# Performance work log

Hardware: AMD Instinct MI355X
Metric: run time of the kernel (lower is better)

## Reference

```python
import jax, jax.numpy as jnp
import numpy as np

B = 2
DIMS = ((41, 800, 800), (21, 400, 400), (11, 200, 200), (6, 100, 100))  # (D,H,W)=(z,y,x) per level
VS = ((0.1, 0.1, 0.2), (0.2, 0.2, 0.4), (0.4, 0.4, 0.8), (0.8, 0.8, 1.6))  # (vx,vy,vz)
OFFSET = (0.0, -40.0, -3.0)  # world offset (x,y,z)
BN_EPS = 1e-3

OFFS27 = jnp.array([[z, y, x] for z in (-1, 0, 1) for y in (-1, 0, 1) for x in (-1, 0, 1)], jnp.int32)

# ---------------- numpy-side input construction ----------------

def _np_downsample(coords, out_dims):
    # active output sites of SparseConv3d(k=3, s=2, p=1): in = 2*o - 1 + kd, kd in 0..2
    outs = []
    for kz in range(3):
        for ky in range(3):
            for kx in range(3):
                o = coords[:, 1:] + 1 - np.array([kz, ky, kx])
                ok = (o % 2 == 0).all(1)
                oc = o // 2
                ok &= (oc >= 0).all(1)
                ok &= (oc[:, 0] < out_dims[0]) & (oc[:, 1] < out_dims[1]) & (oc[:, 2] < out_dims[2])
                outs.append(np.concatenate([coords[ok, :1], oc[ok]], 1))
    return np.unique(np.concatenate(outs, 0), axis=0).astype(np.int32)


def _make_coords(rng):
    per_batch = []
    D0, H0, W0 = DIMS[0]
    for b in range(B):
        nc = 120
        centers = np.stack([rng.integers(3, D0 - 4, nc), rng.integers(5, H0 - 6, nc), rng.integers(5, W0 - 6, nc)], 1)
        offs = rng.integers(-3, 4, (nc, 40, 3))
        p = np.clip((centers[:, None, :] + offs).reshape(-1, 3), 0, np.array(DIMS[0]) - 1)
        p = np.unique(p, axis=0)  # sorted lexicographically == sorted by linear key
        per_batch.append(np.concatenate([np.full((len(p), 1), b), p], 1))
    return np.concatenate(per_batch, 0).astype(np.int32)


def setup_inputs():
    rng = np.random.default_rng(0)
    coords0 = _make_coords(rng)
    coords1 = _np_downsample(coords0, DIMS[1])
    coords2 = _np_downsample(coords1, DIMS[2])
    coords3 = _np_downsample(coords2, DIMS[3])
    n = coords0.shape[0]
    c = coords0.astype(np.float64)
    x = OFFSET[0] + (c[:, 3] + 0.5) * VS[0][0] + rng.uniform(-0.04, 0.04, n)
    y = OFFSET[1] + (c[:, 2] + 0.5) * VS[0][1] + rng.uniform(-0.04, 0.04, n)
    z = OFFSET[2] + (c[:, 1] + 0.5) * VS[0][2] + rng.uniform(-0.08, 0.08, n)
    vf = np.stack([x, y, z, rng.uniform(0.0, 1.0, n)], 1).astype(np.float32)

    def conv_w(k, cin, cout):
        return (rng.standard_normal((k, cin, cout)) / np.sqrt(k * cin)).astype(np.float32)

    def bn_p(ch):
        return np.stack([1.0 + 0.05 * rng.standard_normal(ch), 0.05 * rng.standard_normal(ch)], 0).astype(np.float32)

    inp = dict(voxel_features=vf, coords0=coords0, coords1=coords1, coords2=coords2, coords3=coords3,
               w00=conv_w(27, 4, 16), b00=bn_p(16), w01=conv_w(27, 16, 16), b01=bn_p(16),
               wd0=conv_w(27, 16, 32), bd0=bn_p(32),
               w10=conv_w(27, 32, 32), b10=bn_p(32), w11=conv_w(27, 32, 32), b11=bn_p(32),
               wd1=conv_w(27, 32, 64), bd1=bn_p(64),
               w20=conv_w(27, 64, 64), b20=bn_p(64), w21=conv_w(27, 64, 64), b21=bn_p(64), w22=conv_w(27, 64, 64), b22=bn_p(64),
               wd2=conv_w(27, 64, 64), bd2=bn_p(64),
               w30=conv_w(27, 64, 64), b30=bn_p(64), w31=conv_w(27, 64, 64), b31=bn_p(64), w32=conv_w(27, 64, 64), b32=bn_p(64),
               we=(rng.standard_normal((64, 64)) / 8.0).astype(np.float32), be=bn_p(64),
               fc_w=(rng.standard_normal((64, 160)) / np.sqrt(160.0)).astype(np.float32),
               cls_w=(rng.standard_normal((1, 64)) / 8.0).astype(np.float32),
               reg_w=(rng.standard_normal((3, 64)) / 8.0).astype(np.float32))
    return {k: jnp.asarray(v) for k, v in inp.items()}

# ---------------- jax sparse-conv primitives ----------------

def _key(c, dims):
    D, H, W = dims
    return ((c[:, 0] * D + c[:, 1]) * H + c[:, 2]) * W + c[:, 3]


def _gather(nb_b, nb, feats, keys_sorted, dims):
    # nb: (N,27,3) candidate (z,y,x); gather rows of feats via sorted-key lookup, zeros if absent
    D, H, W = dims
    inb = (nb[..., 0] >= 0) & (nb[..., 0] < D) & (nb[..., 1] >= 0) & (nb[..., 1] < H) & (nb[..., 2] >= 0) & (nb[..., 2] < W)
    nbc = jnp.clip(nb, 0, jnp.array(dims, jnp.int32) - 1)
    qk = ((nb_b * D + nbc[..., 0]) * H + nbc[..., 1]) * W + nbc[..., 2]
    pos = jnp.clip(jnp.searchsorted(keys_sorted, qk), 0, keys_sorted.shape[0] - 1)
    found = inb & (keys_sorted[pos] == qk)
    return jnp.where(found[..., None], feats[pos], 0.0)


def _subm(feats, coords, keys, dims, w):
    nb = coords[:, None, 1:] + OFFS27[None]
    g = _gather(coords[:, None, 0], nb, feats, keys, dims)  # (N,27,Cin)
    return jnp.einsum('nkc,kco->no', g, w)


def _stride(feats, in_keys, in_dims, coords_out, w):
    nb = coords_out[:, None, 1:] * 2 + OFFS27[None]  # in = 2*o - 1 + kd
    g = _gather(coords_out[:, None, 0], nb, feats, in_keys, in_dims)
    return jnp.einsum('nkc,kco->no', g, w)


def _bn_relu(x, p):
    # train-mode BatchNorm1d over active voxels (biased var), eps=1e-3
    m = x.mean(0)
    v = jnp.mean((x - m) ** 2, 0)
    return jax.nn.relu((x - m) * jax.lax.rsqrt(v + BN_EPS) * p[0] + p[1])


def _t2p(coords, vs):
    c = coords.astype(jnp.float32)
    x = OFFSET[0] + (c[:, 3] + 0.5) * vs[0]
    y = OFFSET[1] + (c[:, 2] + 0.5) * vs[1]
    z = OFFSET[2] + (c[:, 1] + 0.5) * vs[2]
    return jnp.stack([c[:, 0], x, y, z], 1)


def _nn_interp(unknown, known, feats):
    # three_nn (squared L2, batch-separated, non-differentiable) + three_interpolate
    d2 = jnp.sum((unknown[:, None, 1:] - known[None, :, 1:]) ** 2, -1)
    d2 = d2 + 1e10 * (unknown[:, None, 0] != known[None, :, 0])
    d2 = jax.lax.stop_gradient(d2)
    negd, idx = jax.lax.top_k(-d2, 3)
    w = 1.0 / (-negd + 1e-8)
    w = w / w.sum(1, keepdims=True)
    return jnp.sum(feats[idx] * w[..., None], 1)


def _forward(voxel_features, w00, b00, w01, b01, wd0, bd0, w10, b10, w11, b11, wd1, bd1,
             w20, b20, w21, b21, w22, b22, wd2, bd2, w30, b30, w31, b31, w32, b32,
             we, be, fc_w, cls_w, reg_w, coords0, coords1, coords2, coords3):
    k0, k1 = _key(coords0, DIMS[0]), _key(coords1, DIMS[1])
    k2 = _key(coords2, DIMS[2])
    points_mean = jnp.concatenate([coords0[:, :1].astype(jnp.float32), voxel_features[:, :3]], 1)
    f = _bn_relu(_subm(voxel_features, coords0, k0, DIMS[0], w00), b00)
    f = _bn_relu(_subm(f, coords0, k0, DIMS[0], w01), b01)
    f = _bn_relu(_stride(f, k0, DIMS[0], coords1, wd0), bd0)
    f = _bn_relu(_subm(f, coords1, k1, DIMS[1], w10), b10)
    f = _bn_relu(_subm(f, coords1, k1, DIMS[1], w11), b11)
    p1 = _nn_interp(points_mean, _t2p(coords1, VS[1]), f)
    f = _bn_relu(_stride(f, k1, DIMS[1], coords2, wd1), bd1)
    f = _bn_relu(_subm(f, coords2, k2, DIMS[2], w20), b20)
    f = _bn_relu(_subm(f, coords2, k2, DIMS[2], w21), b21)
    f = _bn_relu(_subm(f, coords2, k2, DIMS[2], w22), b22)
    p2 = _nn_interp(points_mean, _t2p(coords2, VS[2]), f)
    f = _bn_relu(_stride(f, k2, DIMS[2], coords3, wd2), bd2)
    k3 = _key(coords3, DIMS[3])
    f = _bn_relu(_subm(f, coords3, k3, DIMS[3], w30), b30)
    f = _bn_relu(_subm(f, coords3, k3, DIMS[3], w31), b31)
    f = _bn_relu(_subm(f, coords3, k3, DIMS[3], w32), b32)
    p3 = _nn_interp(points_mean, _t2p(coords3, VS[3]), f)
    out = _bn_relu(f @ we, be)  # extra_conv: 1x1x1 SparseConv3d
    D3, H3, W3 = DIMS[3]
    dense = jnp.zeros((B, D3, H3, W3, 64), out.dtype).at[coords3[:, 0], coords3[:, 1], coords3[:, 2], coords3[:, 3]].set(out)
    xd = dense.transpose(0, 4, 1, 2, 3).reshape(B, 64 * D3, H3, W3)  # (N, C*D, H, W)
    pw = jnp.concatenate([p1, p2, p3], 1) @ fc_w.T
    return (xd, points_mean, pw @ cls_w.T, pw @ reg_w.T)


def reference(voxel_features, w00, b00, w01, b01, wd0, bd0, w10, b10, w11, b11, wd1, bd1,
              w20, b20, w21, b21, w22, b22, wd2, bd2, w30, b30, w31, b31, w32, b32,
              we, be, fc_w, cls_w, reg_w, coords0, coords1, coords2, coords3):
    return _forward(voxel_features, w00, b00, w01, b01, wd0, bd0, w10, b10, w11, b11, wd1, bd1,
                    w20, b20, w21, b21, w22, b22, wd2, bd2, w30, b30, w31, b31, w32, b32,
                    we, be, fc_w, cls_w, reg_w, coords0, coords1, coords2, coords3)
```

## Files before the change

### kernel.cpp

```cpp
#include <hip/hip_runtime.h>

#define OFFX 0.0f
#define OFFY -40.0f
#define OFFZ -3.0f
#define BNEPS 1e-3f
#define NCH 128
#define NG 9

typedef _Float16 h2_t __attribute__((ext_vector_type(2)));
__device__ inline h2_t u2h(unsigned u) { union { unsigned u; h2_t h; } x; x.u = u; return x.h; }
__device__ inline unsigned h2u(h2_t h) { union { unsigned u; h2_t h; } x; x.h = h; return x.u; }

__global__ void keys_k(const int* __restrict__ coords, int n, int D, int H, int W,
                       int* __restrict__ keys) {
  int i = blockIdx.x * 256 + threadIdx.x;
  if (i < n) {
    const int* c = coords + (size_t)i * 4;
    keys[i] = ((c[0] * D + c[1]) * H + c[2]) * W + c[3];
  }
}

__global__ void nbr_k(const int* __restrict__ coords, int np, const int* __restrict__ keys, int nk,
                      int D, int H, int W, int scale, int* __restrict__ nbr) {
  int t = blockIdx.x * 256 + threadIdx.x;
  if (t >= np * 27) return;
  int p = t / 27, k = t % 27;
  int kz = k / 9 - 1, ky = (k / 3) % 3 - 1, kx = k % 3 - 1;
  const int* c = coords + (size_t)p * 4;
  int z = c[1] * scale + kz, y = c[2] * scale + ky, x = c[3] * scale + kx;
  int r = -1;
  if (z >= 0 && z < D && y >= 0 && y < H && x >= 0 && x < W) {
    int q = ((c[0] * D + z) * H + y) * W + x;
    int lo = 0, hi = nk;
    while (lo < hi) { int m = (lo + hi) >> 1; if (keys[m] < q) lo = m + 1; else hi = m; }
    if (lo < nk && keys[lo] == q) r = lo;
  }
  nbr[t] = r;
}

struct WPrep { const float* src; unsigned* dst; int cin; int cout; };
struct WP13 { WPrep l[13]; };
__global__ void wprep_k(WP13 a) {
  WPrep w = a.l[blockIdx.y];
  int cp2 = w.cin / 2;
  int tot = 27 * cp2 * w.cout;
  int i = blockIdx.x * 256 + threadIdx.x;
  if (i >= tot) return;
  int o = i % w.cout, rest = i / w.cout;
  int cp = rest % cp2, k = rest / cp2;
  float lo = w.src[((size_t)k * w.cin + 2 * cp) * w.cout + o];
  float hi = w.src[((size_t)k * w.cin + 2 * cp + 1) * w.cout + o];
  h2_t h; h[0] = (_Float16)lo; h[1] = (_Float16)hi;
  w.dst[i] = h2u(h);
}

template<int CIN, int COUT>
__global__ __launch_bounds__(128) void convg_k(const float* __restrict__ feats,
                                               const int* __restrict__ nbr,
                                               const float* __restrict__ w, int n,
                                               float* __restrict__ partial, int gstride) {
  constexpr int TP = 32;
  constexpr int LDP = 36;
  constexpr int CO = COUT / 16;
  __shared__ float G[CIN * LDP];
  int tid = threadIdx.x;
  int pg = tid >> 4, cg = tid & 15;
  int p0 = blockIdx.x * TP;
  int k0 = blockIdx.y * 3;
  float acc[4][CO];
#pragma unroll
  for (int i = 0; i < 4; i++)
#pragma unroll
    for (int j = 0; j < CO; j++) acc[i][j] = 0.f;

  for (int kk = 0; kk < 3; kk++) {
    int k = k0 + kk;
    __syncthreads();
    for (int ch = tid; ch < TP * CIN / 4; ch += 128) {
      int r = ch & (TP - 1), c4 = ch / TP;
      int p = p0 + r;
      int idx = (p < n) ? nbr[(size_t)p * 27 + k] : -1;
      float4 fv = make_float4(0.f, 0.f, 0.f, 0.f);
      if (idx >= 0) fv = *(const float4*)(feats + (size_t)idx * CIN + c4 * 4);
      G[(c4 * 4 + 0) * LDP + r] = fv.x;
      G[(c4 * 4 + 1) * LDP + r] = fv.y;
      G[(c4 * 4 + 2) * LDP + r] = fv.z;
      G[(c4 * 4 + 3) * LDP + r] = fv.w;
    }
    __syncthreads();
    const float* wk = w + (size_t)k * CIN * COUT + cg * CO;
#pragma unroll
    for (int c = 0; c < CIN; c++) {
      float4 g4 = *(const float4*)&G[c * LDP + pg * 4];
      float wv[CO];
      if constexpr (CO == 4)      *(float4*)wv = *(const float4*)(wk + c * COUT);
      else if constexpr (CO == 2) *(float2*)wv = *(const float2*)(wk + c * COUT);
      else                        wv[0] = wk[c * COUT];
      float gp[4] = {g4.x, g4.y, g4.z, g4.w};
#pragma unroll
      for (int i = 0; i < 4; i++)
#pragma unroll
        for (int j = 0; j < CO; j++) acc[i][j] = fmaf(gp[i], wv[j], acc[i][j]);
    }
  }
#pragma unroll
  for (int i = 0; i < 4; i++) {
    int p = p0 + pg * 4 + i;
    if (p < n) {
      float* dst = partial + (size_t)blockIdx.y * gstride + (size_t)p * COUT + cg * CO;
      if constexpr (CO == 4)      *(float4*)dst = *(float4*)acc[i];
      else if constexpr (CO == 2) *(float2*)dst = *(float2*)acc[i];
      else                        dst[0] = acc[i][0];
    }
  }
}

template<int CIN, int COUT>
__global__ __launch_bounds__(128) void convh_k(const unsigned* __restrict__ fh,
                                               const int* __restrict__ nbr,
                                               const unsigned* __restrict__ wh, int n,
                                               float* __restrict__ partial, int gstride,
                                               const float* __restrict__ scsh) {
  constexpr int TP = 32;
  constexpr int LDPH = 36;
  constexpr int CO = COUT / 16;
  constexpr int CP = CIN / 2;
  __shared__ unsigned H[CP * LDPH];
  int tid = threadIdx.x;
  int pg = tid >> 4, cg = tid & 15;
  int p0 = blockIdx.x * TP;
  int k0 = blockIdx.y * 3;
  int r = tid & 31;
  int p = p0 + r;
  int sidx[3];
  if (p < n) {
    const int* nb = nbr + (size_t)p * 27 + k0;
    sidx[0] = nb[0]; sidx[1] = nb[1]; sidx[2] = nb[2];
  } else { sidx[0] = sidx[1] = sidx[2] = -1; }

  float acc[4][CO];
#pragma unroll
  for (int i = 0; i < 4; i++)
#pragma unroll
    for (int j = 0; j < CO; j++) acc[i][j] = 0.f;

  if constexpr (CIN >= 32) {
    constexpr int NLD = CIN / 32;
    uint4 pf[NLD];
    {
      int idx = sidx[0];
#pragma unroll
      for (int it = 0; it < NLD; it++) {
        int q = (tid >> 5) + it * 4;
        pf[it] = (idx >= 0) ? *(const uint4*)(fh + (size_t)idx * CP + q * 4)
                            : make_uint4(0, 0, 0, 0);
      }
    }
    for (int kk = 0; kk < 3; kk++) {
      bool ok = sidx[kk] >= 0;
      __syncthreads();
#pragma unroll
      for (int it = 0; it < NLD; it++) {
        int q = (tid >> 5) + it * 4;
        unsigned uu[4] = {pf[it].x, pf[it].y, pf[it].z, pf[it].w};
#pragma unroll
        for (int j = 0; j < 4; j++) {
          int cp = q * 4 + j;
          unsigned outw = 0;
          if (ok) {
            h2_t h = u2h(uu[j]);
            float lo = fmaxf(fmaf((float)h[0], scsh[2 * cp], scsh[CIN + 2 * cp]), 0.f);
            float hi = fmaxf(fmaf((float)h[1], scsh[2 * cp + 1], scsh[CIN + 2 * cp + 1]), 0.f);
            h2_t o; o[0] = (_Float16)lo; o[1] = (_Float16)hi;
            outw = h2u(o);
          }
          H[cp * LDPH + r] = outw;
        }
      }
      if (kk < 2) {
        int idx = sidx[kk + 1];
#pragma unroll
        for (int it = 0; it < NLD; it++) {
          int q = (tid >> 5) + it * 4;
          pf[it] = (idx >= 0) ? *(const uint4*)(fh + (size_t)idx * CP + q * 4)
                              : make_uint4(0, 0, 0, 0);
        }
      }
      __syncthreads();
      const unsigned* wk = wh + (size_t)(k0 + kk) * CP * COUT + cg * CO;
#pragma unroll 8
      for (int cp = 0; cp < CP; cp++) {
        uint4 g4 = *(const uint4*)&H[cp * LDPH + pg * 4];
        unsigned gg[4] = {g4.x, g4.y, g4.z, g4.w};
        unsigned wv[CO];
        if constexpr (CO == 4)      *(uint4*)wv = *(const uint4*)(wk + cp * COUT);
        else if constexpr (CO == 2) *(uint2*)wv = *(const uint2*)(wk + cp * COUT);
        else                        wv[0] = wk[cp * COUT];
#pragma unroll
        for (int i = 0; i < 4; i++)
#pragma unroll
          for (int j = 0; j < CO; j++)
            acc[i][j] = __builtin_amdgcn_fdot2(u2h(gg[i]), u2h(wv[j]), acc[i][j], false);
      }
    }
  } else {
    int q = tid >> 5;
    uint2 pf2;
    {
      int idx = sidx[0];
      pf2 = (idx >= 0) ? *(const uint2*)(fh + (size_t)idx * CP + q * 2) : make_uint2(0, 0);
    }
    for (int kk = 0; kk < 3; kk++) {
      bool ok = sidx[kk] >= 0;
      __syncthreads();
      unsigned uu[2] = {pf2.x, pf2.y};
#pragma unroll
      for (int j = 0; j < 2; j++) {
        int cp = q * 2 + j;
        unsigned outw = 0;
        if (ok) {
          h2_t h = u2h(uu[j]);
          float lo = fmaxf(fmaf((float)h[0], scsh[2 * cp], scsh[CIN + 2 * cp]), 0.f);
          float hi = fmaxf(fmaf((float)h[1], scsh[2 * cp + 1], scsh[CIN + 2 * cp + 1]), 0.f);
          h2_t o; o[0] = (_Float16)lo; o[1] = (_Float16)hi;
          outw = h2u(o);
        }
        H[cp * LDPH + r] = outw;
      }
      if (kk < 2) {
        int idx = sidx[kk + 1];
        pf2 = (idx >= 0) ? *(const uint2*)(fh + (size_t)idx * CP + q * 2) : make_uint2(0, 0);
      }
      __syncthreads();
      const unsigned* wk = wh + (size_t)(k0 + kk) * CP * COUT + cg * CO;
#pragma unroll
      for (int cp = 0; cp < CP; cp++) {
        uint4 g4 = *(const uint4*)&H[cp * LDPH + pg * 4];
        unsigned gg[4] = {g4.x, g4.y, g4.z, g4.w};
        unsigned wv[CO];
        if constexpr (CO == 4)      *(uint4*)wv = *(const uint4*)(wk + cp * COUT);
        else if constexpr (CO == 2) *(uint2*)wv = *(const uint2*)(wk + cp * COUT);
        else                        wv[0] = wk[cp * COUT];
#pragma unroll
        for (int i = 0; i < 4; i++)
#pragma unroll
          for (int j = 0; j < CO; j++)
            acc[i][j] = __builtin_amdgcn_fdot2(u2h(gg[i]), u2h(wv[j]), acc[i][j], false);
      }
    }
  }
#pragma unroll
  for (int i = 0; i < 4; i++) {
    int pp = p0 + pg * 4 + i;
    if (pp < n) {
      float* dst = partial + (size_t)blockIdx.y * gstride + (size_t)pp * COUT + cg * CO;
      if constexpr (CO == 4)      *(float4*)dst = *(float4*)acc[i];
      else if constexpr (CO == 2) *(float2*)dst = *(float2*)acc[i];
      else                        dst[0] = acc[i][0];
    }
  }
}

__global__ void bn_k(const float* __restrict__ partial, int G, int gstride, int n, int C,
                     float* __restrict__ pre, unsigned* __restrict__ preh,
                     float* __restrict__ stats, const float* __restrict__ bnp,
                     float* __restrict__ scsh, int* __restrict__ ctr) {
  __shared__ float l1e[256], l2e[256], l1o[256], l2o[256];
  __shared__ int lastf;
  int t = threadIdx.x;
  int total = n * C;
  float s1e = 0.f, s2e = 0.f, s1o = 0.f, s2o = 0.f;
  for (int i2 = (blockIdx.x * 256 + t) * 2; i2 < total; i2 += NCH * 512) {
    float v0 = 0.f, v1 = 0.f;
    for (int g = 0; g < G; g++) {
      float2 pv = *(const float2*)(partial + (size_t)g * gstride + i2);
      v0 += pv.x; v1 += pv.y;
    }
    if (pre) *(float2*)(pre + i2) = make_float2(v0, v1);
    h2_t h; h[0] = (_Float16)v0; h[1] = (_Float16)v1;
    preh[i2 >> 1] = h2u(h);
    s1e += v0; s2e += v0 * v0; s1o += v1; s2o += v1 * v1;
  }
  l1e[t] = s1e; l2e[t] = s2e; l1o[t] = s1o; l2o[t] = s2o;
  for (int s = 128; s >= C / 2; s >>= 1) {
    __syncthreads();
    if (t < s) {
      l1e[t] += l1e[t + s]; l2e[t] += l2e[t + s];
      l1o[t] += l1o[t + s]; l2o[t] += l2o[t + s];
    }
  }
  __syncthreads();
  if (t < C / 2) {
    stats[((size_t)blockIdx.x * C + 2 * t) * 2]     = l1e[t];
    stats[((size_t)blockIdx.x * C + 2 * t) * 2 + 1] = l2e[t];
    stats[((size_t)blockIdx.x * C + 2 * t + 1) * 2]     = l1o[t];
    stats[((size_t)blockIdx.x * C + 2 * t + 1) * 2 + 1] = l2o[t];
  }
  __threadfence();
  __syncthreads();
  if (t == 0) lastf = (atomicAdd(ctr, 1) == NCH - 1) ? 1 : 0;
  __syncthreads();
  if (lastf) {
    __threadfence();
    if (t < C) {
      float a1 = 0.f, a2 = 0.f;
      for (int ch = 0; ch < NCH; ch++) {
        a1 += stats[((size_t)ch * C + t) * 2];
        a2 += stats[((size_t)ch * C + t) * 2 + 1];
      }
      float m = a1 / n;
      float v = a2 / n - m * m;
      float sc = bnp[t] / sqrtf(v + BNEPS);
      scsh[t] = sc;
      scsh[C + t] = bnp[C + t] - m * sc;
    }
  }
}

__global__ void pm_k(const float* __restrict__ vf, const int* __restrict__ c0, int n0,
                     float* __restrict__ pm, float* __restrict__ out1) {
  int i = blockIdx.x * 256 + threadIdx.x;
  if (i >= n0) return;
  float b = (float)c0[(size_t)i * 4];
  float x = vf[(size_t)i * 4], y = vf[(size_t)i * 4 + 1], z = vf[(size_t)i * 4 + 2];
  pm[(size_t)i * 4] = b; pm[(size_t)i * 4 + 1] = x; pm[(size_t)i * 4 + 2] = y; pm[(size_t)i * 4 + 3] = z;
  out1[(size_t)i * 4] = b; out1[(size_t)i * 4 + 1] = x; out1[(size_t)i * 4 + 2] = y; out1[(size_t)i * 4 + 3] = z;
}

__global__ void knnprep_k(const int* __restrict__ coords, int nl, float vx, float vy, float vz,
                          float4* __restrict__ kp4, int* __restrict__ bs) {
  int i = blockIdx.x * 256 + threadIdx.x;
  if (i >= nl) return;
  const int* c = coords + (size_t)i * 4;
  kp4[i] = make_float4(OFFX + (c[3] + 0.5f) * vx,
                       OFFY + (c[2] + 0.5f) * vy,
                       OFFZ + (c[1] + 0.5f) * vz, (float)c[0]);
  if (c[0] == 0 && (i + 1 == nl || coords[(size_t)(i + 1) * 4] == 1)) bs[0] = i + 1;
}

__global__ __launch_bounds__(256) void knn_k(const float4* __restrict__ pm4, int n0,
                                             const float4* __restrict__ kp4, int nl,
                                             const int* __restrict__ bsp,
                                             float* __restrict__ wv, int* __restrict__ iv) {
  __shared__ __align__(16) float4 kp[256];
  __shared__ int bl[4], bh[4];
  int tid = threadIdx.x;
  int wave = tid >> 6, lane = tid & 63;
  int u = blockIdx.x * 4 + wave;
  bool valid = u < n0;
  float4 up = pm4[valid ? u : (n0 - 1)];
  int bs = bsp[0];
  int lo = (up.x == 0.f) ? 0 : bs;
  int hi = (up.x == 0.f) ? bs : nl;
  if (!valid) { lo = 0; hi = 0; }
  if (lane == 0) { bl[wave] = valid ? lo : 0x7fffffff; bh[wave] = valid ? hi : 0; }
  __syncthreads();
  int blo = min(min(bl[0], bl[1]), min(bl[2], bl[3]));
  int bhi = max(max(bh[0], bh[1]), max(bh[2], bh[3]));
  float ux = up.y, uy = up.z, uz = up.w;
  float d0 = 3e38f, d1 = 3e38f, d2 = 3e38f;
  int i0 = -1, i1 = -1, i2 = -1;
#define INS1(DD, GI) { \
    bool l0 = (DD) < d0, l1 = (DD) < d1, l2 = (DD) < d2; \
    i2 = l2 ? (l1 ? i1 : (GI)) : i2; \
    i1 = l1 ? (l0 ? i0 : (GI)) : i1; \
    i0 = l0 ? (GI) : i0; \
    float t1_ = __builtin_amdgcn_fmed3f(d0, d1, (DD)); \
    float t2_ = __builtin_amdgcn_fmed3f(d1, d2, (DD)); \
    d0 = fminf(d0, (DD)); d1 = t1_; d2 = t2_; }
#define DIST(Q) fmaf(ux - (Q).x, ux - (Q).x, fmaf(uy - (Q).y, uy - (Q).y, (uz - (Q).z) * (uz - (Q).z)))
  for (int cb = blo; cb < bhi; cb += 256) {
    int m = bhi - cb; if (m > 256) m = 256;
    __syncthreads();
    if (tid < m) kp[tid] = kp4[cb + tid];
    __syncthreads();
    if (cb + 256 <= lo || cb >= hi) continue;
    if (m == 256 && cb >= lo && cb + 256 <= hi) {
      float4 q0 = kp[lane], q1 = kp[lane + 64], q2 = kp[lane + 128], q3 = kp[lane + 192];
      float a0 = DIST(q0), a1 = DIST(q1), a2 = DIST(q2), a3 = DIST(q3);
      if (__any((a0 < d2) | (a1 < d2) | (a2 < d2) | (a3 < d2))) {
        INS1(a0, cb + lane) INS1(a1, cb + lane + 64)
        INS1(a2, cb + lane + 128) INS1(a3, cb + lane + 192)
      }
    } else {
#pragma unroll
      for (int j = 0; j < 4; j++) {
        int i = lane + 64 * j;
        int e = cb + i;
        if (i < m && e >= lo && e < hi) {
          float4 q = kp[i];
          float dd = DIST(q);
          INS1(dd, e)
        }
      }
    }
  }
#pragma unroll
  for (int off = 1; off < 64; off <<= 1) {
    float e0 = __shfl_xor(d0, off), e1 = __shfl_xor(d1, off), e2 = __shfl_xor(d2, off);
    int j0 = __shfl_xor(i0, off), j1 = __shfl_xor(i1, off), j2 = __shfl_xor(i2, off);
    INS1(e0, j0) INS1(e1, j1) INS1(e2, j2)
  }
#undef DIST
#undef INS1
  if (valid && lane == 0) {
    float w0 = 1.f / (d0 + 1e-8f), w1 = 1.f / (d1 + 1e-8f), w2 = 1.f / (d2 + 1e-8f);
    float s = w0 + w1 + w2;
    wv[(size_t)u * 3] = w0 / s; wv[(size_t)u * 3 + 1] = w1 / s; wv[(size_t)u * 3 + 2] = w2 / s;
    iv[(size_t)u * 3] = i0; iv[(size_t)u * 3 + 1] = i1; iv[(size_t)u * 3 + 2] = i2;
  }
}

__global__ void interp_k(const unsigned* __restrict__ fh, int C, const float* __restrict__ scsh,
                         const float* __restrict__ wv, const int* __restrict__ iv, int n0,
                         float* __restrict__ X, int xoff) {
  int t = blockIdx.x * 256 + threadIdx.x;
  if (t >= n0 * C) return;
  int u = t / C, c = t % C;
  int cp = c >> 1, sel = c & 1;
  int CP = C >> 1;
  float sc = scsh[c], sh = scsh[C + c];
  h2_t h0 = u2h(fh[(size_t)iv[(size_t)u * 3]     * CP + cp]);
  h2_t h1 = u2h(fh[(size_t)iv[(size_t)u * 3 + 1] * CP + cp]);
  h2_t h2v = u2h(fh[(size_t)iv[(size_t)u * 3 + 2] * CP + cp]);
  float a0 = fmaxf(fmaf((float)h0[sel], sc, sh), 0.f);
  float a1 = fmaxf(fmaf((float)h1[sel], sc, sh), 0.f);
  float a2 = fmaxf(fmaf((float)h2v[sel], sc, sh), 0.f);
  X[(size_t)u * 160 + xoff + c] = wv[(size_t)u * 3] * a0 + wv[(size_t)u * 3 + 1] * a1
                                + wv[(size_t)u * 3 + 2] * a2;
}

__global__ __launch_bounds__(256) void conv1x1_k(const unsigned* __restrict__ fh,
                                                 const float* __restrict__ scsh,
                                                 const float* __restrict__ we, int n,
                                                 float* __restrict__ out) {
  __shared__ float rows[256];
  int t = threadIdx.x;
  int p = blockIdx.x * 4 + (t >> 6), c = t & 63;
  float v = 0.f;
  if (p < n) {
    h2_t h = u2h(fh[(size_t)p * 32 + (c >> 1)]);
    v = fmaxf(fmaf((float)h[c & 1], scsh[c], scsh[64 + c]), 0.f);
  }
  rows[t] = v;
  __syncthreads();
  if (p >= n) return;
  const float* fr = rows + (t >> 6) * 64;
  float a = 0.f;
#pragma unroll 16
  for (int ci = 0; ci < 64; ci++) a = fmaf(fr[ci], we[ci * 64 + c], a);
  out[(size_t)p * 64 + c] = a;
}

__global__ void scatter_k(const float* __restrict__ pre, const float* __restrict__ scsh,
                          const int* __restrict__ c3, int n3, float* __restrict__ out0) {
  int t = blockIdx.x * 256 + threadIdx.x;
  if (t >= n3 * 64) return;
  int p = t >> 6, c = t & 63;
  const int* cc = c3 + (size_t)p * 4;
  size_t o = ((((size_t)cc[0] * 64 + c) * 6 + cc[1]) * 100 + cc[2]) * 100 + cc[3];
  out0[o] = fmaxf(fmaf(pre[t], scsh[c], scsh[64 + c]), 0.f);
}

__global__ __launch_bounds__(256) void head_k(const float* __restrict__ X,
                                              const float* __restrict__ fcw,
                                              const float* __restrict__ clsw,
                                              const float* __restrict__ regw,
                                              int n0, float* __restrict__ outc,
                                              float* __restrict__ outr) {
  __shared__ float fl[64 * 161];
  int t = threadIdx.x;
  for (int i = t; i < 64 * 160; i += 256) {
    int r = i / 160, c = i % 160;
    fl[r * 161 + c] = fcw[i];
  }
  __syncthreads();
  int wave = t >> 6, lane = t & 63;
  int u = blockIdx.x * 4 + wave;
  if (u >= n0) return;
  const float* xr = X + (size_t)u * 160;
  const float* wr = fl + (size_t)lane * 161;
  float a = 0.f;
#pragma unroll 8
  for (int i = 0; i < 160; i++) a = fmaf(xr[i], wr[i], a);
  float c = a * clsw[lane];
  float r0 = a * regw[lane], r1 = a * regw[64 + lane], r2 = a * regw[128 + lane];
  for (int off = 32; off; off >>= 1) {
    c  += __shfl_down(c, off);
    r0 += __shfl_down(r0, off);
    r1 += __shfl_down(r1, off);
    r2 += __shfl_down(r2, off);
  }
  if (lane == 0) {
    outc[u] = c;
    outr[(size_t)u * 3] = r0; outr[(size_t)u * 3 + 1] = r1; outr[(size_t)u * 3 + 2] = r2;
  }
}

extern "C" void kernel_launch(void* const* d_in, const int* in_sizes, int n_in,
                              void* d_out, int out_size, void* d_ws, size_t ws_size,
                              hipStream_t stream) {
  const float* vf  = (const float*)d_in[0];
  const int* c0 = (const int*)d_in[1];
  const int* c1 = (const int*)d_in[2];
  const int* c2 = (const int*)d_in[3];
  const int* c3 = (const int*)d_in[4];
  const float* w00 = (const float*)d_in[5];  const float* b00 = (const float*)d_in[6];
  const float* w01 = (const float*)d_in[7];  const float* b01 = (const float*)d_in[8];
  const float* wd0 = (const float*)d_in[9];  const float* bd0 = (const float*)d_in[10];
  const float* w10 = (const float*)d_in[11]; const float* b10 = (const float*)d_in[12];
  const float* w11 = (const float*)d_in[13]; const float* b11 = (const float*)d_in[14];
  const float* wd1 = (const float*)d_in[15]; const float* bd1 = (const float*)d_in[16];
  const float* w20 = (const float*)d_in[17]; const float* b20 = (const float*)d_in[18];
  const float* w21 = (const float*)d_in[19]; const float* b21 = (const float*)d_in[20];
  const float* w22 = (const float*)d_in[21]; const float* b22 = (const float*)d_in[22];
  const float* wd2 = (const float*)d_in[23]; const float* bd2 = (const float*)d_in[24];
  const float* w30 = (const float*)d_in[25]; const float* b30 = (const float*)d_in[26];
  const float* w31 = (const float*)d_in[27]; const float* b31 = (const float*)d_in[28];
  const float* w32 = (const float*)d_in[29]; const float* b32 = (const float*)d_in[30];
  const float* we  = (const float*)d_in[31]; const float* be  = (const float*)d_in[32];
  const float* fcw = (const float*)d_in[33];
  const float* clsw = (const float*)d_in[34];
  const float* regw = (const float*)d_in[35];

  int N0 = in_sizes[1] / 4, N1 = in_sizes[2] / 4, N2 = in_sizes[3] / 4, N3 = in_sizes[4] / 4;
  int maxN = N0; if (N1 > maxN) maxN = N1; if (N2 > maxN) maxN = N2; if (N3 > maxN) maxN = N3;

  auto cdiv = [](int a, int b) { return (a + b - 1) / b; };
  char* p = (char*)d_ws;
  auto alloc = [&](size_t bytes) { char* r = p; p += (bytes + 255) & ~(size_t)255; return r; };

  int* keys0 = (int*)alloc((size_t)N0 * 4);
  int* keys1 = (int*)alloc((size_t)N1 * 4);
  int* keys2 = (int*)alloc((size_t)N2 * 4);
  int* keys3 = (int*)alloc((size_t)N3 * 4);
  int* nbr0  = (int*)alloc((size_t)N0 * 27 * 4);
  int* nbrs1 = (int*)alloc((size_t)N1 * 27 * 4);
  int* nbr1  = (int*)alloc((size_t)N1 * 27 * 4);
  int* nbrs2 = (int*)alloc((size_t)N2 * 27 * 4);
  int* nbr2  = (int*)alloc((size_t)N2 * 27 * 4);
  int* nbrs3 = (int*)alloc((size_t)N3 * 27 * 4);
  int* nbr3  = (int*)alloc((size_t)N3 * 27 * 4);
  float* FA = (float*)alloc((size_t)maxN * 64 * 4);
  float* FB = (float*)alloc((size_t)maxN * 64 * 4);
  float* FC = (float*)alloc((size_t)maxN * 64 * 4);
  unsigned* FAh = (unsigned*)alloc((size_t)maxN * 32 * 4);
  unsigned* FBh = (unsigned*)alloc((size_t)maxN * 32 * 4);
  float* stats = (float*)alloc((size_t)NCH * 64 * 2 * 4);
  float* SC = (float*)alloc((size_t)15 * 128 * 4);
  int* ctrs = (int*)alloc(16 * 4);
  float* wv = (float*)alloc((size_t)N0 * 3 * 4);
  int*   iv = (int*)alloc((size_t)N0 * 3 * 4);
  float* X  = (float*)alloc((size_t)N0 * 160 * 4);
  float* pmb = (float*)alloc((size_t)N0 * 4 * 4);
  float4* kp1 = (float4*)alloc((size_t)N1 * 16);
  float4* kp2 = (float4*)alloc((size_t)N2 * 16);
  float4* kp3 = (float4*)alloc((size_t)N3 * 16);
  int* bsA = (int*)alloc(32);
  unsigned* whbuf = (unsigned*)alloc((size_t)452736 * 4);

  float* out0 = (float*)d_out;
  float* out1 = out0 + 7680000;
  float* outc = out1 + (size_t)N0 * 4;
  float* outr = outc + N0;
  float* partial = out0;

  auto scsh = [&](int L) { return SC + (size_t)L * 128; };

  const float* wsrc[13] = {w01, wd0, w10, w11, wd1, w20, w21, w22, wd2, w30, w31, w32, nullptr};
  int wcin[13]  = {16, 16, 32, 32, 32, 64, 64, 64, 64, 64, 64, 64, 0};
  int wcout[13] = {16, 32, 32, 32, 64, 64, 64, 64, 64, 64, 64, 64, 0};
  unsigned* wdst[13];
  size_t woff = 0;
  WP13 wp{};
  int nw = 12;
  for (int i = 0; i < nw; i++) {
    wdst[i] = whbuf + woff;
    wp.l[i] = WPrep{wsrc[i], wdst[i], wcin[i], wcout[i]};
    woff += (size_t)27 * (wcin[i] / 2) * wcout[i];
  }
  for (int i = nw; i < 13; i++) wp.l[i] = WPrep{w01, wdst[0], 16, 16};

  hipMemsetAsync(ctrs, 0, 16 * 4, stream);
  wprep_k<<<dim3(216, nw), 256, 0, stream>>>(wp);
  keys_k<<<cdiv(N0, 256), 256, 0, stream>>>(c0, N0, 41, 800, 800, keys0);
  keys_k<<<cdiv(N1, 256), 256, 0, stream>>>(c1, N1, 21, 400, 400, keys1);
  keys_k<<<cdiv(N2, 256), 256, 0, stream>>>(c2, N2, 11, 200, 200, keys2);
  keys_k<<<cdiv(N3, 256), 256, 0, stream>>>(c3, N3, 6, 100, 100, keys3);
  nbr_k<<<cdiv(N0 * 27, 256), 256, 0, stream>>>(c0, N0, keys0, N0, 41, 800, 800, 1, nbr0);
  nbr_k<<<cdiv(N1 * 27, 256), 256, 0, stream>>>(c1, N1, keys0, N0, 41, 800, 800, 2, nbrs1);
  nbr_k<<<cdiv(N1 * 27, 256), 256, 0, stream>>>(c1, N1, keys1, N1, 21, 400, 400, 1, nbr1);
  nbr_k<<<cdiv(N2 * 27, 256), 256, 0, stream>>>(c2, N2, keys1, N1, 21, 400, 400, 2, nbrs2);
  nbr_k<<<cdiv(N2 * 27, 256), 256, 0, stream>>>(c2, N2, keys2, N2, 11, 200, 200, 1, nbr2);
  nbr_k<<<cdiv(N3 * 27, 256), 256, 0, stream>>>(c3, N3, keys2, N2, 11, 200, 200, 2, nbrs3);
  nbr_k<<<cdiv(N3 * 27, 256), 256, 0, stream>>>(c3, N3, keys3, N3, 6, 100, 100, 1, nbr3);
  pm_k<<<cdiv(N0, 256), 256, 0, stream>>>(vf, c0, N0, pmb, out1);
  knnprep_k<<<cdiv(N1, 256), 256, 0, stream>>>(c1, N1, 0.2f, 0.2f, 0.4f, kp1, bsA + 0);
  knnprep_k<<<cdiv(N2, 256), 256, 0, stream>>>(c2, N2, 0.4f, 0.4f, 0.8f, kp2, bsA + 1);
  knnprep_k<<<cdiv(N3, 256), 256, 0, stream>>>(c3, N3, 0.8f, 0.8f, 1.6f, kp3, bsA + 2);

  auto convh = [&](const unsigned* fhin, const int* nb, int wi, int n, int cin, int cout,
                   const float* ss) {
    dim3 g(cdiv(n, 32), NG);
    int gs = n * cout;
    const unsigned* wh = wdst[wi];
    if (cin == 16 && cout == 16)
      convh_k<16, 16><<<g, 128, 0, stream>>>(fhin, nb, wh, n, partial, gs, ss);
    else if (cin == 16 && cout == 32)
      convh_k<16, 32><<<g, 128, 0, stream>>>(fhin, nb, wh, n, partial, gs, ss);
    else if (cin == 32 && cout == 32)
      convh_k<32, 32><<<g, 128, 0, stream>>>(fhin, nb, wh, n, partial, gs, ss);
    else if (cin == 32 && cout == 64)
      convh_k<32, 64><<<g, 128, 0, stream>>>(fhin, nb, wh, n, partial, gs, ss);
    else
      convh_k<64, 64><<<g, 128, 0, stream>>>(fhin, nb, wh, n, partial, gs, ss);
  };
  auto bnp = [&](const float* bnpar, int n, int C, float* pre, unsigned* preh, int L) {
    bn_k<<<NCH, 256, 0, stream>>>(partial, NG, n * C, n, C, pre, preh, stats, bnpar,
                                  scsh(L), ctrs + L);
  };
  auto knn = [&](const float4* kp4, const int* bsl, int nl, const unsigned* fh, int C, int L,
                 int xoff) {
    knn_k<<<cdiv(N0, 4), 256, 0, stream>>>((const float4*)pmb, N0, kp4, nl, bsl, wv, iv);
    interp_k<<<cdiv(N0 * C, 256), 256, 0, stream>>>(fh, C, scsh(L), wv, iv, N0, X, xoff);
  };

  convg_k<4, 16><<<dim3(cdiv(N0, 32), NG), 128, 0, stream>>>(vf, nbr0, w00, N0, partial, N0 * 16);
  bnp(b00, N0, 16, nullptr, FAh, 0);
  convh(FAh, nbr0, 0, N0, 16, 16, scsh(0));   bnp(b01, N0, 16, nullptr, FBh, 1);
  convh(FBh, nbrs1, 1, N1, 16, 32, scsh(1));  bnp(bd0, N1, 32, nullptr, FAh, 2);
  convh(FAh, nbr1, 2, N1, 32, 32, scsh(2));   bnp(b10, N1, 32, nullptr, FBh, 3);
  convh(FBh, nbr1, 3, N1, 32, 32, scsh(3));   bnp(b11, N1, 32, nullptr, FAh, 4);
  knn(kp1, bsA + 0, N1, FAh, 32, 4, 0);
  convh(FAh, nbrs2, 4, N2, 32, 64, scsh(4));  bnp(bd1, N2, 64, nullptr, FBh, 5);
  convh(FBh, nbr2, 5, N2, 64, 64, scsh(5));   bnp(b20, N2, 64, nullptr, FAh, 6);
  convh(FAh, nbr2, 6, N2, 64, 64, scsh(6));   bnp(b21, N2, 64, nullptr, FBh, 7);
  convh(FBh, nbr2, 7, N2, 64, 64, scsh(7));   bnp(b22, N2, 64, nullptr, FAh, 8);
  knn(kp2, bsA + 1, N2, FAh, 64, 8, 32);
  convh(FAh, nbrs3, 8, N3, 64, 64, scsh(8));  bnp(bd2, N3, 64, nullptr, FBh, 9);
  convh(FBh, nbr3, 9, N3, 64, 64, scsh(9));   bnp(b30, N3, 64, nullptr, FAh, 10);
  convh(FAh, nbr3, 10, N3, 64, 64, scsh(10)); bnp(b31, N3, 64, nullptr, FBh, 11);
  convh(FBh, nbr3, 11, N3, 64, 64, scsh(11)); bnp(b32, N3, 64, nullptr, FAh, 12);
  knn(kp3, bsA + 2, N3, FAh, 64, 12, 96);

  conv1x1_k<<<cdiv(N3, 4), 256, 0, stream>>>(FAh, scsh(12), we, N3, FC);
  bn_k<<<NCH, 256, 0, stream>>>(FC, 1, 0, N3, 64, FB, FBh, stats, be, scsh(13), ctrs + 13);
  hipMemsetAsync(d_out, 0, (size_t)7680000 * 4, stream);
  scatter_k<<<cdiv(N3 * 64, 256), 256, 0, stream>>>(FB, scsh(13), c3, N3, out0);
  head_k<<<cdiv(N0, 4), 256, 0, stream>>>(X, fcw, clsw, regw, N0, outc, outr);
}
```

Before: 931.2 us.

## Store conv partial sums in fp16 and parallelize BN final stats reduction

Conv kernels with 32 or more output channels now write their per-kernel-group partial sums as packed fp16 pairs instead of fp32. The BN kernel is templated to read either format, which halves partial-buffer traffic for those layers. The last-block BN statistics reduction now spreads the 128 chunk partials across all 256 threads with a shared-memory tree, instead of having C threads loop serially. Rounding partials to fp16 before summation loses some accuracy in the pre-BN values and statistics.

New measurement: 866.0 us. 7.0% less time.

```diff
diff --git a/kernel.cpp b/kernel.cpp
--- a/kernel.cpp
+++ b/kernel.cpp
@@ -119,12 +119,13 @@
 __global__ __launch_bounds__(128) void convh_k(const unsigned* __restrict__ fh,
                                                const int* __restrict__ nbr,
                                                const unsigned* __restrict__ wh, int n,
-                                               float* __restrict__ partial, int gstride,
+                                               void* __restrict__ partial, int gstride,
                                                const float* __restrict__ scsh) {
   constexpr int TP = 32;
   constexpr int LDPH = 36;
   constexpr int CO = COUT / 16;
   constexpr int CP = CIN / 2;
+  constexpr bool H2P = (CO >= 2);
   __shared__ unsigned H[CP * LDPH];
   int tid = threadIdx.x;
   int pg = tid >> 4, cg = tid & 15;
@@ -253,15 +254,28 @@
   for (int i = 0; i < 4; i++) {
     int pp = p0 + pg * 4 + i;
     if (pp < n) {
-      float* dst = partial + (size_t)blockIdx.y * gstride + (size_t)pp * COUT + cg * CO;
-      if constexpr (CO == 4)      *(float4*)dst = *(float4*)acc[i];
-      else if constexpr (CO == 2) *(float2*)dst = *(float2*)acc[i];
-      else                        dst[0] = acc[i][0];
-    }
-  }
-}
-
-__global__ void bn_k(const float* __restrict__ partial, int G, int gstride, int n, int C,
+      if constexpr (H2P) {
+        unsigned* dst = (unsigned*)partial + (size_t)blockIdx.y * gstride
+                      + (size_t)pp * (COUT / 2) + cg * (CO / 2);
+        if constexpr (CO == 4) {
+          h2_t a; a[0] = (_Float16)acc[i][0]; a[1] = (_Float16)acc[i][1];
+          h2_t b; b[0] = (_Float16)acc[i][2]; b[1] = (_Float16)acc[i][3];
+          *(uint2*)dst = make_uint2(h2u(a), h2u(b));
+        } else {
+          h2_t a; a[0] = (_Float16)acc[i][0]; a[1] = (_Float16)acc[i][1];
+          dst[0] = h2u(a);
+        }
+      } else {
+        float* dst = (float*)partial + (size_t)blockIdx.y * gstride
+                   + (size_t)pp * COUT + cg * CO;
+        dst[0] = acc[i][0];
+      }
+    }
+  }
+}
+
+template<bool H2P>
+__global__ void bn_k(const void* __restrict__ partial, int G, int gstride, int n, int C,
                      float* __restrict__ pre, unsigned* __restrict__ preh,
                      float* __restrict__ stats, const float* __restrict__ bnp,
                      float* __restrict__ scsh, int* __restrict__ ctr) {
@@ -272,9 +286,18 @@
   float s1e = 0.f, s2e = 0.f, s1o = 0.f, s2o = 0.f;
   for (int i2 = (blockIdx.x * 256 + t) * 2; i2 < total; i2 += NCH * 512) {
     float v0 = 0.f, v1 = 0.f;
-    for (int g = 0; g < G; g++) {
-      float2 pv = *(const float2*)(partial + (size_t)g * gstride + i2);
-      v0 += pv.x; v1 += pv.y;
+    if constexpr (H2P) {
+      const unsigned* ph = (const unsigned*)partial;
+      for (int g = 0; g < G; g++) {
+        h2_t h = u2h(ph[(size_t)g * gstride + (i2 >> 1)]);
+        v0 += (float)h[0]; v1 += (float)h[1];
+      }
+    } else {
+      const float* pf = (const float*)partial;
+      for (int g = 0; g < G; g++) {
+        float2 pv = *(const float2*)(pf + (size_t)g * gstride + i2);
+        v0 += pv.x; v1 += pv.y;
+      }
     }
     if (pre) *(float2*)(pre + i2) = make_float2(v0, v1);
     h2_t h; h[0] = (_Float16)v0; h[1] = (_Float16)v1;
@@ -302,14 +325,22 @@
   __syncthreads();
   if (lastf) {
     __threadfence();
+    int c = t % C, sub = t / C;
+    int TPC = 256 / C;
+    float a1 = 0.f, a2 = 0.f;
+    for (int ch = sub; ch < NCH; ch += TPC) {
+      a1 += stats[((size_t)ch * C + c) * 2];
+      a2 += stats[((size_t)ch * C + c) * 2 + 1];
+    }
+    l1e[t] = a1; l2e[t] = a2;
+    for (int s = 128; s >= C; s >>= 1) {
+      __syncthreads();
+      if (t < s) { l1e[t] += l1e[t + s]; l2e[t] += l2e[t + s]; }
+    }
+    __syncthreads();
     if (t < C) {
-      float a1 = 0.f, a2 = 0.f;
-      for (int ch = 0; ch < NCH; ch++) {
-        a1 += stats[((size_t)ch * C + t) * 2];
-        a2 += stats[((size_t)ch * C + t) * 2 + 1];
-      }
-      float m = a1 / n;
-      float v = a2 / n - m * m;
+      float m = l1e[t] / n;
+      float v = l2e[t] / n - m * m;
       float sc = bnp[t] / sqrtf(v + BNEPS);
       scsh[t] = sc;
       scsh[C + t] = bnp[C + t] - m * sc;
@@ -563,7 +594,7 @@
   float* out1 = out0 + 7680000;
   float* outc = out1 + (size_t)N0 * 4;
   float* outr = outc + N0;
-  float* partial = out0;
+  void* partial = out0;
 
   auto scsh = [&](int L) { return SC + (size_t)L * 128; };
 
@@ -602,7 +633,7 @@
   auto convh = [&](const unsigned* fhin, const int* nb, int wi, int n, int cin, int cout,
                    const float* ss) {
     dim3 g(cdiv(n, 32), NG);
-    int gs = n * cout;
+    int gs = (cout >= 32) ? n * cout / 2 : n * cout;
     const unsigned* wh = wdst[wi];
     if (cin == 16 && cout == 16)
       convh_k<16, 16><<<g, 128, 0, stream>>>(fhin, nb, wh, n, partial, gs, ss);
@@ -615,9 +646,14 @@
     else
       convh_k<64, 64><<<g, 128, 0, stream>>>(fhin, nb, wh, n, partial, gs, ss);
   };
-  auto bnp = [&](const float* bnpar, int n, int C, float* pre, unsigned* preh, int L) {
-    bn_k<<<NCH, 256, 0, stream>>>(partial, NG, n * C, n, C, pre, preh, stats, bnpar,
-                                  scsh(L), ctrs + L);
+  auto bnp = [&](const float* bnpar, int n, int C, float* pre, unsigned* preh, int L, bool h2p) {
+    int gs = h2p ? n * C / 2 : n * C;
+    if (h2p)
+      bn_k<true><<<NCH, 256, 0, stream>>>(partial, NG, gs, n, C, pre, preh, stats, bnpar,
+                                          scsh(L), ctrs + L);
+    else
+      bn_k<false><<<NCH, 256, 0, stream>>>(partial, NG, gs, n, C, pre, preh, stats, bnpar,
+                                           scsh(L), ctrs + L);
   };
   auto knn = [&](const float4* kp4, const int* bsl, int nl, const unsigned* fh, int C, int L,
                  int xoff) {
@@ -625,26 +661,28 @@
     interp_k<<<cdiv(N0 * C, 256), 256, 0, stream>>>(fh, C, scsh(L), wv, iv, N0, X, xoff);
   };
 
-  convg_k<4, 16><<<dim3(cdiv(N0, 32), NG), 128, 0, stream>>>(vf, nbr0, w00, N0, partial, N0 * 16);
-  bnp(b00, N0, 16, nullptr, FAh, 0);
-  convh(FAh, nbr0, 0, N0, 16, 16, scsh(0));   bnp(b01, N0, 16, nullptr, FBh, 1);
-  convh(FBh, nbrs1, 1, N1, 16, 32, scsh(1));  bnp(bd0, N1, 32, nullptr, FAh, 2);
-  convh(FAh, nbr1, 2, N1, 32, 32, scsh(2));   bnp(b10, N1, 32, nullptr, FBh, 3);
-  convh(FBh, nbr1, 3, N1, 32, 32, scsh(3));   bnp(b11, N1, 32, nullptr, FAh, 4);
+  convg_k<4, 16><<<dim3(cdiv(N0, 32), NG), 128, 0, stream>>>(vf, nbr0, w00, N0,
+                                                             (float*)partial, N0 * 16);
+  bnp(b00, N0, 16, nullptr, FAh, 0, false);
+  convh(FAh, nbr0, 0, N0, 16, 16, scsh(0));   bnp(b01, N0, 16, nullptr, FBh, 1, false);
+  convh(FBh, nbrs1, 1, N1, 16, 32, scsh(1));  bnp(bd0, N1, 32, nullptr, FAh, 2, true);
+  convh(FAh, nbr1, 2, N1, 32, 32, scsh(2));   bnp(b10, N1, 32, nullptr, FBh, 3, true);
+  convh(FBh, nbr1, 3, N1, 32, 32, scsh(3));   bnp(b11, N1, 32, nullptr, FAh, 4, true);
   knn(kp1, bsA + 0, N1, FAh, 32, 4, 0);
-  convh(FAh, nbrs2, 4, N2, 32, 64, scsh(4));  bnp(bd1, N2, 64, nullptr, FBh, 5);
-  convh(FBh, nbr2, 5, N2, 64, 64, scsh(5));   bnp(b20, N2, 64, nullptr, FAh, 6);
-  convh(FAh, nbr2, 6, N2, 64, 64, scsh(6));   bnp(b21, N2, 64, nullptr, FBh, 7);
-  convh(FBh, nbr2, 7, N2, 64, 64, scsh(7));   bnp(b22, N2, 64, nullptr, FAh, 8);
+  convh(FAh, nbrs2, 4, N2, 32, 64, scsh(4));  bnp(bd1, N2, 64, nullptr, FBh, 5, true);
+  convh(FBh, nbr2, 5, N2, 64, 64, scsh(5));   bnp(b20, N2, 64, nullptr, FAh, 6, true);
+  convh(FAh, nbr2, 6, N2, 64, 64, scsh(6));   bnp(b21, N2, 64, nullptr, FBh, 7, true);
+  convh(FBh, nbr2, 7, N2, 64, 64, scsh(7));   bnp(b22, N2, 64, nullptr, FAh, 8, true);
   knn(kp2, bsA + 1, N2, FAh, 64, 8, 32);
-  convh(FAh, nbrs3, 8, N3, 64, 64, scsh(8));  bnp(bd2, N3, 64, nullptr, FBh, 9);
-  convh(FBh, nbr3, 9, N3, 64, 64, scsh(9));   bnp(b30, N3, 64, nullptr, FAh, 10);
-  convh(FAh, nbr3, 10, N3, 64, 64, scsh(10)); bnp(b31, N3, 64, nullptr, FBh, 11);
-  convh(FBh, nbr3, 11, N3, 64, 64, scsh(11)); bnp(b32, N3, 64, nullptr, FAh, 12);
+  convh(FAh, nbrs3, 8, N3, 64, 64, scsh(8));  bnp(bd2, N3, 64, nullptr, FBh, 9, true);
+  convh(FBh, nbr3, 9, N3, 64, 64, scsh(9));   bnp(b30, N3, 64, nullptr, FAh, 10, true);
+  convh(FAh, nbr3, 10, N3, 64, 64, scsh(10)); bnp(b31, N3, 64, nullptr, FBh, 11, true);
+  convh(FBh, nbr3, 11, N3, 64, 64, scsh(11)); bnp(b32, N3, 64, nullptr, FAh, 12, true);
   knn(kp3, bsA + 2, N3, FAh, 64, 12, 96);
 
   conv1x1_k<<<cdiv(N3, 4), 256, 0, stream>>>(FAh, scsh(12), we, N3, FC);
-  bn_k<<<NCH, 256, 0, stream>>>(FC, 1, 0, N3, 64, FB, FBh, stats, be, scsh(13), ctrs + 13);
+  bn_k<false><<<NCH, 256, 0, stream>>>(FC, 1, 0, N3, 64, FB, FBh, stats, be, scsh(13),
+                                       ctrs + 13);
   hipMemsetAsync(d_out, 0, (size_t)7680000 * 4, stream);
   scatter_k<<<cdiv(N3 * 64, 256), 256, 0, stream>>>(FB, scsh(13), c3, N3, out0);
   head_k<<<cdiv(N0, 4), 256, 0, stream>>>(X, fcw, clsw, regw, N0, outc, outr);
```
